# Optimization experiments

Measured on AMD Instinct MI355X. Metric: run time of the kernel, lower is better.

The kernel has to match this reference:

```python
import jax, jax.numpy as jnp
import numpy as np

B, IN, OUT = 256, 512, 512


def setup_inputs() -> dict:
    key = jax.random.key(0)
    k0, k1, k2, k3, k4, k5 = jax.random.split(key, 6)
    x_mean = jax.random.normal(k0, (B, IN), jnp.float32)
    x_var = jax.random.normal(k1, (B, IN, IN), jnp.float32)
    # params (original inits A_mean to zeros which gives a degenerate test;
    # use small random values for a meaningful numerical baseline)
    xavier_std = float(np.sqrt(2.0 / (IN + OUT)))
    A_mean = jax.random.normal(k2, (IN, OUT), jnp.float32) * xavier_std
    A_var = jax.random.normal(k3, (IN, OUT), jnp.float32) * xavier_std
    b_mean = jax.random.normal(k4, (OUT,), jnp.float32) * 0.01
    b_var = jax.random.normal(k5, (OUT,), jnp.float32)
    return {"x_mean": x_mean, "x_var": x_var, "A_mean": A_mean,
            "A_var": A_var, "b_mean": b_mean, "b_var": b_var}


def reference(x_mean, x_var, A_mean, A_var, b_mean, b_var):
    # y_mean = x A_mean + b_mean   (F.linear(x, A.t()) == x @ A)
    y_mean = x_mean @ A_mean + b_mean  # [B, OUT]

    # E[x x] diagonal: Var[x]_ii + mean_i^2
    x_var_diag = jnp.diagonal(x_var, axis1=1, axis2=2)  # [B, IN]
    xx_mean = x_var_diag + x_mean * x_mean
    term1_diag = xx_mean @ A_var  # [B, OUT]

    # A^T Cov[x] A, full matrix as in original, then take its diagonal
    xCov_A = jnp.einsum('bij,jo->bio', x_var, A_mean)      # [B, IN, OUT]
    A_xCov_A = jnp.einsum('bio,ip->bop', xCov_A, A_mean)   # [B, OUT, OUT]
    term2_diag = jnp.diagonal(A_xCov_A, axis1=1, axis2=2)  # [B, OUT]

    result_diag = term1_diag + term2_diag + b_var
    y_var = jax.vmap(jnp.diag)(result_diag)  # diag_embed -> [B, OUT, OUT]
    return y_mean, y_var
```

## Files before the change

kernel.cpp:

```cpp
#include <hip/hip_runtime.h>
#include <hip/hip_bf16.h>


typedef __bf16 bf16x8 __attribute__((ext_vector_type(8)));
typedef float f32x4 __attribute__((ext_vector_type(4)));

__device__ inline ushort f2bf(float f) {
    union { float f; unsigned u; } x; x.f = f;
    unsigned u = x.u + 0x7fffu + ((x.u >> 16) & 1u);
    return (ushort)(u >> 16);
}

__device__ inline void gload16(const void* g, void* l) {
    __builtin_amdgcn_global_load_lds(
        (const __attribute__((address_space(1))) void*)g,
        (__attribute__((address_space(3))) void*)l, 16, 0, 0);
}

__global__ void k_prep_at(const float* __restrict__ am, ushort* __restrict__ abt) {
    int C = blockIdx.x * 256 + threadIdx.x;
    int nt = C >> 13;
    int L  = C & 8191;
    int ks = L >> 9;
    int rem = L & 511;
    int s = rem >> 3, c = rem & 7;
    int lc = c ^ (s & 7);
    int h = lc >> 2, g = lc & 3;
    int r = 2 * s + h;
    int o = nt * 128 + r;
    int j0 = ks * 32 + g * 8;
    ushort u[8];
    #pragma unroll
    for (int e = 0; e < 8; ++e) u[e] = f2bf(am[(j0 + e) * 512 + o]);
    *(int4*)(abt + (long)C * 8) = *(int4*)u;
}

__global__ void k_diag(const float* __restrict__ xv, const float* __restrict__ xm,
                       float* __restrict__ xx) {
    int idx = blockIdx.x * 256 + threadIdx.x;
    int b = idx >> 9, i = idx & 511;
    float m = xm[idx];
    xx[idx] = xv[(long)b * 262144 + i * 513] + m * m;
}

__global__ void k_t1(const float* __restrict__ xm, const float* __restrict__ xx,
                     const float* __restrict__ am, const float* __restrict__ av,
                     float* __restrict__ yp, float* __restrict__ tp) {
    __shared__ float S[2][64];
    int t = threadIdx.x;
    int b  = blockIdx.x >> 3;
    int ic = blockIdx.x & 7;
    int i0 = ic * 64;
    if (t < 128) {
        int which = t >> 6, ii = t & 63;
        const float* src = which ? xx : xm;
        S[which][ii] = src[b * 512 + i0 + ii];
    }
    __syncthreads();
    int mat = t >> 7;
    int o4 = t & 127;
    const float* M = mat ? av : am;
    const float* Sv = S[mat];
    f32x4 acc = {0.f, 0.f, 0.f, 0.f};
    #pragma unroll 8
    for (int ii = 0; ii < 64; ++ii) {
        f32x4 a = *(const f32x4*)(M + (long)(i0 + ii) * 512 + o4 * 4);
        float s = Sv[ii];
        acc[0] = fmaf(s, a[0], acc[0]);
        acc[1] = fmaf(s, a[1], acc[1]);
        acc[2] = fmaf(s, a[2], acc[2]);
        acc[3] = fmaf(s, a[3], acc[3]);
    }
    float* dst = (mat ? tp : yp) + ((long)ic * 256 + b) * 512 + o4 * 4;
    *(f32x4*)dst = acc;
}

__global__ __launch_bounds__(256, 3) void k_gemm2(
        const float*  __restrict__ xv,
        const ushort* __restrict__ abt,
        const float*  __restrict__ amean,
        float* __restrict__ p2,
        float* __restrict__ yvar)
{
    __shared__ float  ldsX[2][4096];
    __shared__ ushort ldsA[2][4096];
    __shared__ float  red[2][128];

    int t = threadIdx.x;
    int lane = t & 63;
    int wave = t >> 6;
    int wm = wave >> 1, wn = wave & 1;

    int bid = blockIdx.x;
    int swz = (bid & 7) * 512 + (bid >> 3);
    int mtile = swz >> 2;
    int ntile = swz & 3;
    int n0 = ntile * 128;
    long m0 = (long)mtile * 128;
    int msub = mtile & 3;
    int b = mtile >> 2;

    f32x4 acc[4][4];
    #pragma unroll
    for (int a = 0; a < 4; ++a)
        #pragma unroll
        for (int bq = 0; bq < 4; ++bq)
            acc[a][bq] = (f32x4){0.f, 0.f, 0.f, 0.f};

    const float* xs0 = xv + (m0 + wave * 32 + (lane >> 3)) * 512
                       + ((lane & 7) ^ (lane >> 3)) * 4;
    const char* as0 = (const char*)abt + (long)ntile * 131072
                      + wave * 2048 + lane * 16;

    auto stage = [&](int buf, int ks) {
        char* xd = (char*)(&ldsX[buf][0]) + wave * 4096;
        const float* sx = xs0 + ks * 32;
        #pragma unroll
        for (int q = 0; q < 4; ++q)
            gload16(sx + q * 8 * 512, xd + q * 1024);
        char* ad = (char*)(&ldsA[buf][0]) + wave * 2048;
        const char* sa = as0 + (long)ks * 8192;
        gload16(sa, ad);
        gload16(sa + 1024, ad + 1024);
    };

    auto compute = [&](int buf) {
        bf16x8 af[4], bfr[4];
        int g = lane >> 4;
        #pragma unroll
        for (int nf = 0; nf < 4; ++nf) {
            int r = wn * 64 + nf * 16 + (lane & 15);
            int s = r >> 1;
            int chunk = (((r & 1) << 2) | g) ^ (s & 7);
            bfr[nf] = *(const bf16x8*)((const char*)(&ldsA[buf][0])
                                       + s * 128 + (chunk << 4));
        }
        #pragma unroll
        for (int mf = 0; mf < 4; ++mf) {
            int r = wm * 64 + mf * 16 + (lane & 15);
            int sw = r & 7;
            const char* bx = (const char*)(&ldsX[buf][0]) + r * 128;
            f32x4 lo = *(const f32x4*)(bx + (((2 * g) ^ sw) << 4));
            f32x4 hi = *(const f32x4*)(bx + (((2 * g + 1) ^ sw) << 4));
            bf16x8 a;
            a[0] = (__bf16)lo[0]; a[1] = (__bf16)lo[1];
            a[2] = (__bf16)lo[2]; a[3] = (__bf16)lo[3];
            a[4] = (__bf16)hi[0]; a[5] = (__bf16)hi[1];
            a[6] = (__bf16)hi[2]; a[7] = (__bf16)hi[3];
            af[mf] = a;
        }
        #pragma unroll
        for (int mf = 0; mf < 4; ++mf)
            #pragma unroll
            for (int nf = 0; nf < 4; ++nf)
                acc[mf][nf] = __builtin_amdgcn_mfma_f32_16x16x32_bf16(
                    af[mf], bfr[nf], acc[mf][nf], 0, 0, 0);
    };

    stage(0, 0);
    int cur = 0;
    #pragma unroll
    for (int ks = 0; ks < 16; ++ks) {
        if (ks < 15) stage(cur ^ 1, ks + 1);
        if (ks < 15) asm volatile("s_waitcnt vmcnt(6)" ::: "memory");
        else         asm volatile("s_waitcnt vmcnt(0)" ::: "memory");
        __builtin_amdgcn_s_barrier();
        __builtin_amdgcn_sched_barrier(0);
        compute(cur);
        __builtin_amdgcn_sched_barrier(0);
        __builtin_amdgcn_s_barrier();
        cur ^= 1;
    }

    #pragma unroll
    for (int nf = 0; nf < 4; ++nf) {
        float p = 0.f;
        int o = n0 + wn * 64 + nf * 16 + (lane & 15);
        #pragma unroll
        for (int mf = 0; mf < 4; ++mf) {
            #pragma unroll
            for (int j = 0; j < 4; ++j) {
                int i = msub * 128 + wm * 64 + mf * 16 + ((lane >> 4) * 4) + j;
                p += acc[mf][nf][j] * amean[i * 512 + o];
            }
        }
        p += __shfl_xor(p, 16, 64);
        p += __shfl_xor(p, 32, 64);
        if (lane < 16) red[wm][wn * 64 + nf * 16 + lane] = p;
    }
    __syncthreads();
    if (t < 128) {
        float v = red[0][t] + red[1][t];
        p2[((long)b * 4 + msub) * 512 + n0 + t] = v;
    }

    {
        float* zb = yvar + ((long)b * 512 + msub * 128 + ntile * 32) * 512 + t * 4;
        float4 z = make_float4(0.f, 0.f, 0.f, 0.f);
        #pragma unroll
        for (int q = 0; q < 16; ++q)
            *(float4*)(zb + (long)q * 1024) = z;
    }
}

__global__ void k_final(const float* __restrict__ yp, const float* __restrict__ tp,
                        const float* __restrict__ p2,
                        const float* __restrict__ bm, const float* __restrict__ bv,
                        float* __restrict__ ymean, float* __restrict__ yvar) {
    int idx = blockIdx.x * 256 + threadIdx.x;
    int b = idx >> 9, o = idx & 511;
    float ym = bm[o], t1 = bv[o];
    #pragma unroll
    for (int ic = 0; ic < 8; ++ic) {
        ym += yp[((long)ic * 256 + b) * 512 + o];
        t1 += tp[((long)ic * 256 + b) * 512 + o];
    }
    long pb = (long)b * 2048 + o;
    t1 += p2[pb] + p2[pb + 512] + p2[pb + 1024] + p2[pb + 1536];
    ymean[idx] = ym;
    yvar[(long)idx * 512 + o] = t1;
}

extern "C" void kernel_launch(void* const* d_in, const int* in_sizes, int n_in,
                              void* d_out, int out_size, void* d_ws, size_t ws_size,
                              hipStream_t stream) {
    const float* x_mean = (const float*)d_in[0];
    const float* x_var  = (const float*)d_in[1];
    const float* A_mean = (const float*)d_in[2];
    const float* A_var  = (const float*)d_in[3];
    const float* b_mean = (const float*)d_in[4];
    const float* b_var  = (const float*)d_in[5];

    float* ymean = (float*)d_out;
    float* yvar  = (float*)d_out + 131072;

    char* ws = (char*)d_ws;
    ushort* abt = (ushort*)ws;
    float*  p2  = (float*)(ws + 512 * 1024);
    float*  yp  = (float*)(ws + 2560 * 1024);
    float*  tp  = (float*)(ws + 6656 * 1024);
    float*  xx  = (float*)(ws + 10752 * 1024);

    k_prep_at<<<128, 256, 0, stream>>>(A_mean, abt);
    k_diag<<<512, 256, 0, stream>>>(x_var, x_mean, xx);
    k_t1<<<2048, 256, 0, stream>>>(x_mean, xx, A_mean, A_var, yp, tp);
    k_gemm2<<<4096, 256, 0, stream>>>(x_var, abt, A_mean, p2, yvar);
    k_final<<<512, 256, 0, stream>>>(yp, tp, p2, b_mean, b_var, ymean, yvar);
}
```

Measured before the change: 220.7 us.

## Single-buffer LDS in GEMM kernel to double occupancy and interleave zero-fill stores

Drops the double-buffered LDS pipeline in the main GEMM kernel and uses one buffer with plain __syncthreads around each stage/compute step. It raises launch bounds from 3 to 6 blocks per CU, relying on the halved LDS footprint and more resident waves to hide load latency. The zeroing stores for the diagonal output are moved into the K loop so they overlap with compute. The risk is register pressure at the higher occupancy target, which could cause spills. The loop also loses the explicit prefetch overlap within each block.

Measured after the change: 721.3 us. +226.8%, slower.

```diff
diff --git a/kernel.cpp b/kernel.cpp
--- a/kernel.cpp
+++ b/kernel.cpp
@@ -75,15 +75,15 @@
     *(f32x4*)dst = acc;
 }
 
-__global__ __launch_bounds__(256, 3) void k_gemm2(
+__global__ __launch_bounds__(256, 6) void k_gemm2(
         const float*  __restrict__ xv,
         const ushort* __restrict__ abt,
         const float*  __restrict__ amean,
         float* __restrict__ p2,
         float* __restrict__ yvar)
 {
-    __shared__ float  ldsX[2][4096];
-    __shared__ ushort ldsA[2][4096];
+    __shared__ float  ldsX[4096];
+    __shared__ ushort ldsA[4096];
     __shared__ float  red[2][128];
 
     int t = threadIdx.x;
@@ -112,19 +112,19 @@
     const char* as0 = (const char*)abt + (long)ntile * 131072
                       + wave * 2048 + lane * 16;
 
-    auto stage = [&](int buf, int ks) {
-        char* xd = (char*)(&ldsX[buf][0]) + wave * 4096;
+    auto stage = [&](int ks) {
+        char* xd = (char*)ldsX + wave * 4096;
         const float* sx = xs0 + ks * 32;
         #pragma unroll
         for (int q = 0; q < 4; ++q)
             gload16(sx + q * 8 * 512, xd + q * 1024);
-        char* ad = (char*)(&ldsA[buf][0]) + wave * 2048;
+        char* ad = (char*)ldsA + wave * 2048;
         const char* sa = as0 + (long)ks * 8192;
         gload16(sa, ad);
         gload16(sa + 1024, ad + 1024);
     };
 
-    auto compute = [&](int buf) {
+    auto compute = [&]() {
         bf16x8 af[4], bfr[4];
         int g = lane >> 4;
         #pragma unroll
@@ -132,14 +132,13 @@
             int r = wn * 64 + nf * 16 + (lane & 15);
             int s = r >> 1;
             int chunk = (((r & 1) << 2) | g) ^ (s & 7);
-            bfr[nf] = *(const bf16x8*)((const char*)(&ldsA[buf][0])
-                                       + s * 128 + (chunk << 4));
+            bfr[nf] = *(const bf16x8*)((const char*)ldsA + s * 128 + (chunk << 4));
         }
         #pragma unroll
         for (int mf = 0; mf < 4; ++mf) {
             int r = wm * 64 + mf * 16 + (lane & 15);
             int sw = r & 7;
-            const char* bx = (const char*)(&ldsX[buf][0]) + r * 128;
+            const char* bx = (const char*)ldsX + r * 128;
             f32x4 lo = *(const f32x4*)(bx + (((2 * g) ^ sw) << 4));
             f32x4 hi = *(const f32x4*)(bx + (((2 * g + 1) ^ sw) << 4));
             bf16x8 a;
@@ -157,19 +156,15 @@
                     af[mf], bfr[nf], acc[mf][nf], 0, 0, 0);
     };
 
-    stage(0, 0);
-    int cur = 0;
-    #pragma unroll
+    float* zb = yvar + ((long)b * 512 + msub * 128 + ntile * 32) * 512 + t * 4;
+    float4 z = make_float4(0.f, 0.f, 0.f, 0.f);
+
     for (int ks = 0; ks < 16; ++ks) {
-        if (ks < 15) stage(cur ^ 1, ks + 1);
-        if (ks < 15) asm volatile("s_waitcnt vmcnt(6)" ::: "memory");
-        else         asm volatile("s_waitcnt vmcnt(0)" ::: "memory");
-        __builtin_amdgcn_s_barrier();
-        __builtin_amdgcn_sched_barrier(0);
-        compute(cur);
-        __builtin_amdgcn_sched_barrier(0);
-        __builtin_amdgcn_s_barrier();
-        cur ^= 1;
+        stage(ks);
+        __syncthreads();
+        *(float4*)(zb + (long)ks * 1024) = z;
+        compute();
+        __syncthreads();
     }
 
     #pragma unroll
@@ -193,14 +188,6 @@
         float v = red[0][t] + red[1][t];
         p2[((long)b * 4 + msub) * 512 + n0 + t] = v;
     }
-
-    {
-        float* zb = yvar + ((long)b * 512 + msub * 128 + ntile * 32) * 512 + t * 4;
-        float4 z = make_float4(0.f, 0.f, 0.f, 0.f);
-        #pragma unroll
-        for (int q = 0; q < 16; ++q)
-            *(float4*)(zb + (long)q * 1024) = z;
-    }
 }
 
 __global__ void k_final(const float* __restrict__ yp, const float* __restrict__ tp,
```
